# Kernel tuning notes

Measured on AMD Instinct MI355X. Metric: run time of the kernel, lower is better.

The kernel has to match this reference:

```python
import jax, jax.numpy as jnp
import numpy as np

NX = 96
N_NODES = 6 * NX * NX          # 55296 cubed-sphere grid points
N_EDGES = 4 * N_NODES          # ~4-neighbor connectivity
HID = 32
NUM_STEPS = 3


def setup_inputs() -> dict:
    key = jax.random.key(0)
    ks = jax.random.split(key, 12)
    s = 0.05
    inp = {
        "in_node_features": jax.random.normal(ks[0], (2, 6, NX, NX, 32), jnp.float32),
        "edge_relation": jax.random.normal(ks[1], (N_EDGES, 4), jnp.float32),
        "pw1": jax.random.normal(ks[2], (32, HID), jnp.float32) * s,
        "pb1": jnp.zeros((HID,), jnp.float32),
        "pw2": jax.random.normal(ks[3], (HID, HID), jnp.float32) * s,
        "pb2": jnp.zeros((HID,), jnp.float32),
        "ew1": jax.random.normal(ks[4], (4, 32), jnp.float32) * s,
        "eb1": jnp.zeros((32,), jnp.float32),
        "ew2": jax.random.normal(ks[5], (32, HID * HID), jnp.float32) * s,
        "eb2": jnp.zeros((HID * HID,), jnp.float32),
        "conv_b": jnp.zeros((HID,), jnp.float32),
        "gru_w_ih": jax.random.normal(ks[6], (3 * HID, HID), jnp.float32) * s,
        "gru_w_hh": jax.random.normal(ks[7], (3 * HID, HID), jnp.float32) * s,
        "gru_b_ih": jnp.zeros((3 * HID,), jnp.float32),
        "gru_b_hh": jnp.zeros((3 * HID,), jnp.float32),
        "edge_src": jax.random.randint(ks[8], (N_EDGES,), 0, N_NODES, jnp.int32),
        "edge_dst": jax.random.randint(ks[9], (N_EDGES,), 0, N_NODES, jnp.int32),
    }
    return inp


def reference(in_node_features, edge_relation, pw1, pb1, pw2, pb2,
              ew1, eb1, ew2, eb2, conv_b,
              gru_w_ih, gru_w_hh, gru_b_ih, gru_b_hh,
              edge_src, edge_dst):
    B, T, nx1, nx2, C = in_node_features.shape
    N = T * nx1 * nx2
    H = pw2.shape[1]

    x = in_node_features.reshape(B, N, C)
    # project_node_features: Linear -> ReLU -> Linear
    h0 = jnp.maximum(x @ pw1 + pb1, 0.0) @ pw2 + pb2          # [B, N, H]

    # edge network (same every step): Linear -> ReLU -> Linear -> [E, H, H]
    We = (jnp.maximum(edge_relation @ ew1 + eb1, 0.0) @ ew2 + eb2)
    We = We.reshape(-1, H, H)                                  # [E, H, H]

    def seg_sum(m):  # m: [E, H] -> [N, H]
        return jax.ops.segment_sum(m, edge_dst, num_segments=N)

    def step(carry, _):
        node, hidden = carry                                   # each [B, N, H]
        # NNConv: gather src feats, per-edge matmul, scatter-sum to dst
        msg = jnp.einsum('beh,eho->beo', node[:, edge_src], We)  # [B, E, H]
        agg = jax.vmap(seg_sum)(msg) + conv_b                    # [B, N, H]
        node = jnp.maximum(agg, 0.0)                             # ReLU
        # single GRU step (seq_len = 1)
        gx = node @ gru_w_ih.T + gru_b_ih                        # [B, N, 3H]
        gh = hidden @ gru_w_hh.T + gru_b_hh
        r = jax.nn.sigmoid(gx[..., :H] + gh[..., :H])
        z = jax.nn.sigmoid(gx[..., H:2 * H] + gh[..., H:2 * H])
        n = jnp.tanh(gx[..., 2 * H:] + r * gh[..., 2 * H:])
        hidden = (1.0 - z) * n + z * hidden
        return (hidden, hidden), None

    (node, _), _ = jax.lax.scan(step, (h0, h0), None, length=NUM_STEPS)
    return node.reshape(B, T, nx1, nx2, H)
```

## Files before the change

### kernel.cpp

```cpp
#include <hip/hip_runtime.h>

typedef unsigned short u16;
typedef short s16x8 __attribute__((ext_vector_type(8)));
typedef float f32x4 __attribute__((ext_vector_type(4)));
typedef float f32x2 __attribute__((ext_vector_type(2)));

#define NNODES 55296
#define NEDGES 221184
#define ROWS   110592
#define NBLK_SCAN 216

#define PK_FMA(acc, a, b) \
    asm("v_pk_fma_f32 %0, %1, %2, %0" : "+v"(acc) : "v"(a), "v"(b))

__device__ __forceinline__ u16 f2bf(float f) {
    union { float f; unsigned u; } v; v.f = f;
    unsigned r = (v.u + 0x7fffu + ((v.u >> 16) & 1u)) >> 16;
    return (u16)r;
}
__device__ __forceinline__ float bf2f(u16 u) {
    return __uint_as_float(((unsigned)u) << 16);
}

__global__ __launch_bounds__(256) void hist_kernel(
    const int* __restrict__ edst, int* __restrict__ cnt)
{
    int i = blockIdx.x * 256 + threadIdx.x;
    atomicAdd(&cnt[edst[i]], 1);
}

__global__ __launch_bounds__(256) void scan1_kernel(
    const int* __restrict__ cnt, int* __restrict__ exc, int* __restrict__ bsum)
{
    __shared__ int s[256];
    int t = threadIdx.x, g = blockIdx.x * 256 + t;
    int v = cnt[g];
    s[t] = v; __syncthreads();
#pragma unroll
    for (int d = 1; d < 256; d <<= 1) {
        int x = (t >= d) ? s[t - d] : 0;
        __syncthreads();
        s[t] += x;
        __syncthreads();
    }
    exc[g] = s[t] - v;
    if (t == 255) bsum[blockIdx.x] = s[255];
}

__global__ __launch_bounds__(256) void scan2_kernel(
    const int* __restrict__ bsum, int* __restrict__ bofs)
{
    __shared__ int s[256];
    int t = threadIdx.x;
    int v = (t < NBLK_SCAN) ? bsum[t] : 0;
    s[t] = v; __syncthreads();
#pragma unroll
    for (int d = 1; d < 256; d <<= 1) {
        int x = (t >= d) ? s[t - d] : 0;
        __syncthreads();
        s[t] += x;
        __syncthreads();
    }
    if (t < NBLK_SCAN) bofs[t] = s[t] - v;
}

__global__ __launch_bounds__(256) void scatter_kernel(
    const int* __restrict__ edst, const int* __restrict__ esrc,
    const int* __restrict__ exc, const int* __restrict__ bofs,
    int* __restrict__ cnt,
    int* __restrict__ perm, int* __restrict__ esrcp, int* __restrict__ edstp)
{
    int i = blockIdx.x * 256 + threadIdx.x;
    int d = edst[i];
    int slot = atomicSub(&cnt[d], 1) - 1;
    int pos = exc[d] + bofs[d >> 8] + slot;
    perm[pos] = i;
    esrcp[pos] = esrc[i];
    edstp[pos] = d;
}

__global__ __launch_bounds__(256) void pack_all(
    const float* __restrict__ ew2, u16* __restrict__ ew2f,
    const float* __restrict__ pw1, u16* __restrict__ pw1h, u16* __restrict__ pw1l,
    const float* __restrict__ pw2, u16* __restrict__ pw2h, u16* __restrict__ pw2l,
    const float* __restrict__ wih, u16* __restrict__ wihh, u16* __restrict__ wihl,
    const float* __restrict__ whh, u16* __restrict__ whhh, u16* __restrict__ whhl)
{
    int b = blockIdx.x;
    const float* src; u16 *hi, *lo; int ncols, trans, base;
    if (b < 128)      { src = ew2; hi = ew2f; lo = nullptr; ncols = 1024; trans = 0; base = 0;   }
    else if (b < 132) { src = pw1; hi = pw1h; lo = pw1l;    ncols = 32;   trans = 0; base = 128; }
    else if (b < 136) { src = pw2; hi = pw2h; lo = pw2l;    ncols = 32;   trans = 0; base = 132; }
    else if (b < 148) { src = wih; hi = wihh; lo = wihl;    ncols = 96;   trans = 1; base = 136; }
    else              { src = whh; hi = whhh; lo = whhl;    ncols = 96;   trans = 1; base = 148; }
    int idx = (b - base) * 256 + threadIdx.x;
    int t = idx >> 9, rr = idx & 511, lane = rr >> 3, j = rr & 7;
    int k = (lane >> 4) * 8 + j;
    int n = t * 16 + (lane & 15);
    float v = trans ? src[n * 32 + k] : src[k * ncols + n];
    u16 hb = f2bf(v);
    hi[idx] = hb;
    if (lo) lo[idx] = f2bf(v - bf2f(hb));
}

__global__ __launch_bounds__(256) void edgemlp_kernel(
    const float* __restrict__ er, const float* __restrict__ ew1,
    const float* __restrict__ eb1, const int* __restrict__ perm,
    u16* __restrict__ rbf)
{
    __shared__ float er_lds[128];
    __shared__ float w_lds[128];
    __shared__ float b_lds[32];
    int tid = threadIdx.x;
    int e32 = blockIdx.x * 32;
    if (tid < 128) {
        int e = perm[e32 + (tid >> 2)];
        er_lds[tid] = er[e * 4 + (tid & 3)];
    } else {
        w_lds[tid - 128] = ew1[tid - 128];
    }
    if (tid < 32) b_lds[tid] = eb1[tid];
    __syncthreads();
    int el0 = tid >> 5, o = tid & 31;
    float bo = b_lds[o];
    float w0 = w_lds[o], w1 = w_lds[32 + o], w2 = w_lds[64 + o], w3 = w_lds[96 + o];
#pragma unroll
    for (int i = 0; i < 4; ++i) {
        int el = el0 + i * 8;
        const float* e4 = er_lds + el * 4;
        float v = bo + e4[0] * w0 + e4[1] * w1 + e4[2] * w2 + e4[3] * w3;
        rbf[(e32 + el) * 32 + o] = f2bf(fmaxf(v, 0.f));
    }
}

__global__ __launch_bounds__(256) void nodeproj_kernel(
    const float* __restrict__ x,
    const u16* __restrict__ pw1h, const u16* __restrict__ pw1l, const float* __restrict__ pb1,
    const u16* __restrict__ pw2h, const u16* __restrict__ pw2l, const float* __restrict__ pb2,
    float* __restrict__ st_f32, float* __restrict__ agg)
{
    __shared__ alignas(16) u16 t_hi[4][512];
    __shared__ alignas(16) u16 t_lo[4][512];
    int tid = threadIdx.x, wave = tid >> 6, lane = tid & 63;
    int quad = lane >> 4, col = lane & 15;
    int row0 = (blockIdx.x * 4 + wave) * 16;

    {
        f32x4 z = {0,0,0,0};
        float* zp = agg + (size_t)(row0 + col) * 32 + quad * 8;
        *(f32x4*)(zp) = z; *(f32x4*)(zp + 4) = z;
    }

    const float* xp = x + (size_t)(row0 + col) * 32 + quad * 8;
    f32x4 xv0 = *(const f32x4*)(xp), xv1 = *(const f32x4*)(xp + 4);
    s16x8 ah, al;
#pragma unroll
    for (int i = 0; i < 4; ++i) {
        u16 h0 = f2bf(xv0[i]); ah[i] = (short)h0; al[i] = (short)f2bf(xv0[i] - bf2f(h0));
        u16 h1 = f2bf(xv1[i]); ah[4+i] = (short)h1; al[4+i] = (short)f2bf(xv1[i] - bf2f(h1));
    }
#pragma unroll
    for (int t = 0; t < 2; ++t) {
        s16x8 bh = *(const s16x8*)(pw1h + t * 512 + lane * 8);
        s16x8 bl = *(const s16x8*)(pw1l + t * 512 + lane * 8);
        f32x4 acc = {0,0,0,0};
        acc = __builtin_amdgcn_mfma_f32_16x16x32_bf16(al, bh, acc, 0,0,0);
        acc = __builtin_amdgcn_mfma_f32_16x16x32_bf16(ah, bl, acc, 0,0,0);
        acc = __builtin_amdgcn_mfma_f32_16x16x32_bf16(ah, bh, acc, 0,0,0);
        float bias = pb1[t * 16 + col];
#pragma unroll
        for (int r = 0; r < 4; ++r) {
            float v = fmaxf(acc[r] + bias, 0.f);
            u16 hb = f2bf(v);
            int idx = (quad * 4 + r) * 32 + t * 16 + col;
            t_hi[wave][idx] = hb;
            t_lo[wave][idx] = f2bf(v - bf2f(hb));
        }
    }
    __syncthreads();
    s16x8 th = *(const s16x8*)(&t_hi[wave][col * 32 + quad * 8]);
    s16x8 tl = *(const s16x8*)(&t_lo[wave][col * 32 + quad * 8]);
#pragma unroll
    for (int t = 0; t < 2; ++t) {
        s16x8 bh = *(const s16x8*)(pw2h + t * 512 + lane * 8);
        s16x8 bl = *(const s16x8*)(pw2l + t * 512 + lane * 8);
        f32x4 acc = {0,0,0,0};
        acc = __builtin_amdgcn_mfma_f32_16x16x32_bf16(tl, bh, acc, 0,0,0);
        acc = __builtin_amdgcn_mfma_f32_16x16x32_bf16(th, bl, acc, 0,0,0);
        acc = __builtin_amdgcn_mfma_f32_16x16x32_bf16(th, bh, acc, 0,0,0);
        float bias = pb2[t * 16 + col];
#pragma unroll
        for (int r = 0; r < 4; ++r) {
            float v = acc[r] + bias;
            int row = row0 + quad * 4 + r;
            int o = t * 16 + col;
            st_f32[(size_t)row * 32 + o] = v;
        }
    }
}

__global__ __launch_bounds__(256) void msg_kernel(
    const u16* __restrict__ rbf, const u16* __restrict__ ew2f,
    const float* __restrict__ eb2, const float* __restrict__ state,
    const int* __restrict__ esrcp, const int* __restrict__ edstp,
    float* __restrict__ agg)
{
    __shared__ alignas(16) float eb2_lds[1024];
    __shared__ alignas(16) float ns_lds[4][64 * 18];
    int tid = threadIdx.x;
    {
        *(f32x4*)(eb2_lds + tid * 4) = *(const f32x4*)(eb2 + tid * 4);
    }
    int wave = tid >> 6, lane = tid & 63;
    int quad = lane >> 4, col = lane & 15;
    int e0 = (blockIdx.x * 4 + wave) * 16;

    s16x8 afrag = *(const s16x8*)(rbf + (size_t)(e0 + col) * 32 + quad * 8);

    {
        int el = lane >> 2, part = lane & 3;
        int b = part >> 1, hhalf = part & 1;
        int src = esrcp[e0 + el];
        const float* sp = state + (size_t)(b * NNODES + src) * 32 + hhalf * 16;
        f32x4 a0 = *(const f32x4*)(sp + 0);
        f32x4 a1 = *(const f32x4*)(sp + 4);
        f32x4 a2 = *(const f32x4*)(sp + 8);
        f32x4 a3 = *(const f32x4*)(sp + 12);
        float* wb = &ns_lds[wave][(b * 32 + hhalf * 16) * 18 + el];
        wb[0*18] = a0.x; wb[1*18] = a0.y; wb[2*18] = a0.z; wb[3*18] = a0.w;
        wb[4*18] = a1.x; wb[5*18] = a1.y; wb[6*18] = a1.z; wb[7*18] = a1.w;
        wb[8*18] = a2.x; wb[9*18] = a2.y; wb[10*18] = a2.z; wb[11*18] = a2.w;
        wb[12*18] = a3.x; wb[13*18] = a3.y; wb[14*18] = a3.z; wb[15*18] = a3.w;
    }
    int dstid[4];
#pragma unroll
    for (int r = 0; r < 4; ++r) dstid[r] = edstp[e0 + quad * 4 + r];
    __syncthreads();

    f32x2 m[2][2][2];
#pragma unroll
    for (int b = 0; b < 2; ++b)
#pragma unroll
        for (int oh = 0; oh < 2; ++oh)
#pragma unroll
            for (int p = 0; p < 2; ++p) m[b][oh][p] = f32x2{0.f, 0.f};

    const float* nsw = &ns_lds[wave][0];
    int ep = quad * 4;
#pragma unroll 4
    for (int hh = 0; hh < 16; ++hh) {
        int h0 = hh * 2, h1 = hh * 2 + 1;
        s16x8 b0 = *(const s16x8*)(ew2f + (4 * hh + 0) * 512 + lane * 8);
        s16x8 b1 = *(const s16x8*)(ew2f + (4 * hh + 1) * 512 + lane * 8);
        s16x8 b2 = *(const s16x8*)(ew2f + (4 * hh + 2) * 512 + lane * 8);
        s16x8 b3 = *(const s16x8*)(ew2f + (4 * hh + 3) * 512 + lane * 8);
        float e00 = eb2_lds[h0 * 32 + col],  e01 = eb2_lds[h0 * 32 + 16 + col];
        float e10 = eb2_lds[h1 * 32 + col],  e11 = eb2_lds[h1 * 32 + 16 + col];
        f32x4 c0 = {e00, e00, e00, e00};
        f32x4 c1 = {e01, e01, e01, e01};
        f32x4 c2 = {e10, e10, e10, e10};
        f32x4 c3 = {e11, e11, e11, e11};
        f32x4 d0 = __builtin_amdgcn_mfma_f32_16x16x32_bf16(afrag, b0, c0, 0,0,0);
        f32x4 d1 = __builtin_amdgcn_mfma_f32_16x16x32_bf16(afrag, b1, c1, 0,0,0);
        f32x4 d2 = __builtin_amdgcn_mfma_f32_16x16x32_bf16(afrag, b2, c2, 0,0,0);
        f32x4 d3 = __builtin_amdgcn_mfma_f32_16x16x32_bf16(afrag, b3, c3, 0,0,0);
        f32x2 d0l = __builtin_shufflevector(d0, d0, 0, 1), d0h = __builtin_shufflevector(d0, d0, 2, 3);
        f32x2 d1l = __builtin_shufflevector(d1, d1, 0, 1), d1h = __builtin_shufflevector(d1, d1, 2, 3);
        f32x2 d2l = __builtin_shufflevector(d2, d2, 0, 1), d2h = __builtin_shufflevector(d2, d2, 2, 3);
        f32x2 d3l = __builtin_shufflevector(d3, d3, 0, 1), d3h = __builtin_shufflevector(d3, d3, 2, 3);
        const float* r00 = nsw + (0 * 32 + h0) * 18 + ep;
        const float* r01 = nsw + (0 * 32 + h1) * 18 + ep;
        const float* r10 = nsw + (1 * 32 + h0) * 18 + ep;
        const float* r11 = nsw + (1 * 32 + h1) * 18 + ep;
        f32x2 n00a = *(const f32x2*)(r00), n00b = *(const f32x2*)(r00 + 2);
        f32x2 n01a = *(const f32x2*)(r01), n01b = *(const f32x2*)(r01 + 2);
        f32x2 n10a = *(const f32x2*)(r10), n10b = *(const f32x2*)(r10 + 2);
        f32x2 n11a = *(const f32x2*)(r11), n11b = *(const f32x2*)(r11 + 2);
        PK_FMA(m[0][0][0], n00a, d0l); PK_FMA(m[0][0][0], n01a, d2l);
        PK_FMA(m[0][0][1], n00b, d0h); PK_FMA(m[0][0][1], n01b, d2h);
        PK_FMA(m[0][1][0], n00a, d1l); PK_FMA(m[0][1][0], n01a, d3l);
        PK_FMA(m[0][1][1], n00b, d1h); PK_FMA(m[0][1][1], n01b, d3h);
        PK_FMA(m[1][0][0], n10a, d0l); PK_FMA(m[1][0][0], n11a, d2l);
        PK_FMA(m[1][0][1], n10b, d0h); PK_FMA(m[1][0][1], n11b, d2h);
        PK_FMA(m[1][1][0], n10a, d1l); PK_FMA(m[1][1][0], n11a, d3l);
        PK_FMA(m[1][1][1], n10b, d1h); PK_FMA(m[1][1][1], n11b, d3h);
    }
    float msgs[2][2][4];
#pragma unroll
    for (int b = 0; b < 2; ++b)
#pragma unroll
        for (int oh = 0; oh < 2; ++oh) {
            msgs[b][oh][0] = m[b][oh][0].x; msgs[b][oh][1] = m[b][oh][0].y;
            msgs[b][oh][2] = m[b][oh][1].x; msgs[b][oh][3] = m[b][oh][1].y;
        }
    bool valid[4] = {true, true, true, true};
#pragma unroll
    for (int r = 3; r >= 1; --r) {
        if (dstid[r] == dstid[r - 1]) {
            valid[r] = false;
            msgs[0][0][r-1] += msgs[0][0][r];
            msgs[0][1][r-1] += msgs[0][1][r];
            msgs[1][0][r-1] += msgs[1][0][r];
            msgs[1][1][r-1] += msgs[1][1][r];
        }
    }
#pragma unroll
    for (int r = 0; r < 4; ++r) {
        if (valid[r]) {
#pragma unroll
            for (int b = 0; b < 2; ++b) {
                float* base = agg + ((size_t)b * NNODES + dstid[r]) * 32;
                unsafeAtomicAdd(base + col,      msgs[b][0][r]);
                unsafeAtomicAdd(base + 16 + col, msgs[b][1][r]);
            }
        }
    }
}

__global__ __launch_bounds__(256) void gru_kernel(
    float* __restrict__ agg, const float* __restrict__ conv_b,
    const float* __restrict__ st_f32,
    const u16* __restrict__ wihh, const u16* __restrict__ wihl,
    const u16* __restrict__ whhh, const u16* __restrict__ whhl,
    const float* __restrict__ b_ih, const float* __restrict__ b_hh,
    float* __restrict__ out_f32, int zero_agg)
{
    int tid = threadIdx.x, wave = tid >> 6, lane = tid & 63;
    int quad = lane >> 4, col = lane & 15;
    int row0 = (blockIdx.x * 4 + wave) * 16;

    float* ap = agg + (size_t)(row0 + col) * 32 + quad * 8;
    f32x4 av0 = *(const f32x4*)(ap), av1 = *(const f32x4*)(ap + 4);
    if (zero_agg) {
        f32x4 z = {0,0,0,0};
        *(f32x4*)(ap) = z; *(f32x4*)(ap + 4) = z;
    }
    const float* cb = conv_b + quad * 8;
    f32x4 cb0 = *(const f32x4*)(cb), cb1 = *(const f32x4*)(cb + 4);
    s16x8 anh, anl;
#pragma unroll
    for (int i = 0; i < 4; ++i) {
        float v0 = fmaxf(av0[i] + cb0[i], 0.f);
        float v1 = fmaxf(av1[i] + cb1[i], 0.f);
        u16 h0 = f2bf(v0); anh[i] = (short)h0;   anl[i] = (short)f2bf(v0 - bf2f(h0));
        u16 h1 = f2bf(v1); anh[4+i] = (short)h1; anl[4+i] = (short)f2bf(v1 - bf2f(h1));
    }
    const float* hp = st_f32 + (size_t)(row0 + col) * 32 + quad * 8;
    f32x4 hv0 = *(const f32x4*)(hp), hv1 = *(const f32x4*)(hp + 4);
    s16x8 ahh, ahl;
#pragma unroll
    for (int i = 0; i < 4; ++i) {
        u16 h0 = f2bf(hv0[i]); ahh[i] = (short)h0;   ahl[i] = (short)f2bf(hv0[i] - bf2f(h0));
        u16 h1 = f2bf(hv1[i]); ahh[4+i] = (short)h1; ahl[4+i] = (short)f2bf(hv1[i] - bf2f(h1));
    }

    f32x4 gx[6], gh[6];
#pragma unroll
    for (int t = 0; t < 6; ++t) {
        s16x8 bh = *(const s16x8*)(wihh + t * 512 + lane * 8);
        s16x8 bl = *(const s16x8*)(wihl + t * 512 + lane * 8);
        f32x4 acc = {0,0,0,0};
        acc = __builtin_amdgcn_mfma_f32_16x16x32_bf16(anl, bh, acc, 0,0,0);
        acc = __builtin_amdgcn_mfma_f32_16x16x32_bf16(anh, bl, acc, 0,0,0);
        acc = __builtin_amdgcn_mfma_f32_16x16x32_bf16(anh, bh, acc, 0,0,0);
        gx[t] = acc;
        s16x8 ch = *(const s16x8*)(whhh + t * 512 + lane * 8);
        s16x8 cl = *(const s16x8*)(whhl + t * 512 + lane * 8);
        f32x4 acc2 = {0,0,0,0};
        acc2 = __builtin_amdgcn_mfma_f32_16x16x32_bf16(ahl, ch, acc2, 0,0,0);
        acc2 = __builtin_amdgcn_mfma_f32_16x16x32_bf16(ahh, cl, acc2, 0,0,0);
        acc2 = __builtin_amdgcn_mfma_f32_16x16x32_bf16(ahh, ch, acc2, 0,0,0);
        gh[t] = acc2;
    }
    float bihv[6], bhhv[6];
#pragma unroll
    for (int t = 0; t < 6; ++t) { bihv[t] = b_ih[t * 16 + col]; bhhv[t] = b_hh[t * 16 + col]; }

#pragma unroll
    for (int r = 0; r < 4; ++r) {
        int row = row0 + quad * 4 + r;
#pragma unroll
        for (int oh = 0; oh < 2; ++oh) {
            int o = oh * 16 + col;
            float hid = st_f32[(size_t)row * 32 + o];
            float sr = (gx[oh][r] + bihv[oh]) + (gh[oh][r] + bhhv[oh]);
            float sz = (gx[2+oh][r] + bihv[2+oh]) + (gh[2+oh][r] + bhhv[2+oh]);
            float gxn = gx[4+oh][r] + bihv[4+oh];
            float ghn = gh[4+oh][r] + bhhv[4+oh];
            float rr = 1.f / (1.f + __expf(-sr));
            float zz = 1.f / (1.f + __expf(-sz));
            float narg = gxn + rr * ghn;
            float ex = __expf(2.f * narg);
            float nn = (ex - 1.f) / (ex + 1.f);
            float hnew = (1.f - zz) * nn + zz * hid;
            out_f32[(size_t)row * 32 + o] = hnew;
        }
    }
}

extern "C" void kernel_launch(void* const* d_in, const int* in_sizes, int n_in,
                              void* d_out, int out_size, void* d_ws, size_t ws_size,
                              hipStream_t stream)
{
    const float* x      = (const float*)d_in[0];
    const float* er     = (const float*)d_in[1];
    const float* pw1    = (const float*)d_in[2];
    const float* pb1    = (const float*)d_in[3];
    const float* pw2    = (const float*)d_in[4];
    const float* pb2    = (const float*)d_in[5];
    const float* ew1    = (const float*)d_in[6];
    const float* eb1    = (const float*)d_in[7];
    const float* ew2    = (const float*)d_in[8];
    const float* eb2    = (const float*)d_in[9];
    const float* conv_b = (const float*)d_in[10];
    const float* wih    = (const float*)d_in[11];
    const float* whh    = (const float*)d_in[12];
    const float* bih    = (const float*)d_in[13];
    const float* bhh    = (const float*)d_in[14];
    const int*   esrc   = (const int*)d_in[15];
    const int*   edst   = (const int*)d_in[16];
    float* out = (float*)d_out;

    char* ws = (char*)d_ws;
    size_t off = 0;
    auto alloc = [&](size_t bytes) -> void* {
        void* p = ws + off;
        off = (off + bytes + 255) & ~(size_t)255;
        return p;
    };
    u16*   rbf    = (u16*)  alloc((size_t)(NEDGES + 32) * 32 * 2);
    float* st_f32 = (float*)alloc((size_t)ROWS * 32 * 4);
    float* agg    = (float*)alloc((size_t)ROWS * 32 * 4);
    u16*   ew2f   = (u16*)  alloc(64 * 512 * 2);
    u16*   pw1h   = (u16*)  alloc(2 * 512 * 2);
    u16*   pw1l   = (u16*)  alloc(2 * 512 * 2);
    u16*   pw2h   = (u16*)  alloc(2 * 512 * 2);
    u16*   pw2l   = (u16*)  alloc(2 * 512 * 2);
    u16*   wihhf  = (u16*)  alloc(6 * 512 * 2);
    u16*   wihlf  = (u16*)  alloc(6 * 512 * 2);
    u16*   whhhf  = (u16*)  alloc(6 * 512 * 2);
    u16*   whhlf  = (u16*)  alloc(6 * 512 * 2);
    int*   cnt      = (int*)alloc((size_t)NNODES * 4);
    int*   exc      = (int*)alloc((size_t)NNODES * 4);
    int*   bsum     = (int*)alloc(NBLK_SCAN * 4);
    int*   bofs     = (int*)alloc(NBLK_SCAN * 4);
    int*   perm     = (int*)alloc((size_t)NEDGES * 4);
    int*   esrcp    = (int*)alloc((size_t)(NEDGES + 32) * 4);
    int*   edstp    = (int*)alloc((size_t)(NEDGES + 32) * 4);
    (void)in_sizes; (void)n_in; (void)out_size; (void)ws_size;

    hipMemsetAsync(cnt, 0, (size_t)NNODES * 4, stream);
    hist_kernel<<<NEDGES / 256, 256, 0, stream>>>(edst, cnt);
    scan1_kernel<<<NBLK_SCAN, 256, 0, stream>>>(cnt, exc, bsum);
    scan2_kernel<<<1, 256, 0, stream>>>(bsum, bofs);
    scatter_kernel<<<NEDGES / 256, 256, 0, stream>>>(edst, esrc, exc, bofs, cnt,
                                                     perm, esrcp, edstp);

    pack_all<<<160, 256, 0, stream>>>(ew2, ew2f, pw1, pw1h, pw1l, pw2, pw2h, pw2l,
                                      wih, wihhf, wihlf, whh, whhhf, whhlf);

    edgemlp_kernel<<<NEDGES / 32, 256, 0, stream>>>(er, ew1, eb1, perm, rbf);
    nodeproj_kernel<<<ROWS / 64, 256, 0, stream>>>(x, pw1h, pw1l, pb1, pw2h, pw2l, pb2,
                                                   st_f32, agg);
    for (int s = 0; s < 3; ++s) {
        msg_kernel<<<NEDGES / 64, 256, 0, stream>>>(rbf, ew2f, eb2, st_f32,
                                                    esrcp, edstp, agg);
        float* of = (s == 2) ? out : st_f32;
        gru_kernel<<<ROWS / 64, 256, 0, stream>>>(agg, conv_b, st_f32,
                                                  wihhf, wihlf, whhhf, whhlf, bih, bhh,
                                                  of, (s < 2) ? 1 : 0);
    }
}
```

Baseline: 346.2 us.

## Fuse weight packing into histogram and edge MLP into CSR scatter

Weight packing moves into the histogram kernel and the edge MLP moves into the scatter kernel, which now computes each edge's hidden row from a coalesced read and writes it straight to its sorted position. This drops two launches and the perm array with its indirect gather. It also changes the LDS layout of gathered node states in the message kernel, adding per-part offsets, which looks aimed at reducing bank conflicts. In exchange, the scatter kernel now writes 64-byte rbf rows to scattered positions.

```diff
diff --git a/kernel.cpp b/kernel.cpp
--- a/kernel.cpp
+++ b/kernel.cpp
@@ -1,9 +1,11 @@
 #include <hip/hip_runtime.h>
 
 typedef unsigned short u16;
+typedef unsigned int u32;
 typedef short s16x8 __attribute__((ext_vector_type(8)));
 typedef float f32x4 __attribute__((ext_vector_type(4)));
 typedef float f32x2 __attribute__((ext_vector_type(2)));
+typedef u32 u32x4 __attribute__((ext_vector_type(4)));
 
 #define NNODES 55296
 #define NEDGES 221184
@@ -22,11 +24,34 @@
     return __uint_as_float(((unsigned)u) << 16);
 }
 
-__global__ __launch_bounds__(256) void hist_kernel(
-    const int* __restrict__ edst, int* __restrict__ cnt)
+__global__ __launch_bounds__(256) void hist_pack_kernel(
+    const int* __restrict__ edst, int* __restrict__ cnt,
+    const float* __restrict__ ew2, u16* __restrict__ ew2f,
+    const float* __restrict__ pw1, u16* __restrict__ pw1h, u16* __restrict__ pw1l,
+    const float* __restrict__ pw2, u16* __restrict__ pw2h, u16* __restrict__ pw2l,
+    const float* __restrict__ wih, u16* __restrict__ wihh, u16* __restrict__ wihl,
+    const float* __restrict__ whh, u16* __restrict__ whhh, u16* __restrict__ whhl)
 {
     int i = blockIdx.x * 256 + threadIdx.x;
     atomicAdd(&cnt[edst[i]], 1);
+
+    int b = blockIdx.x;
+    if (b < 160) {
+        const float* src; u16 *hi, *lo; int ncols, trans, base;
+        if (b < 128)      { src = ew2; hi = ew2f; lo = nullptr; ncols = 1024; trans = 0; base = 0;   }
+        else if (b < 132) { src = pw1; hi = pw1h; lo = pw1l;    ncols = 32;   trans = 0; base = 128; }
+        else if (b < 136) { src = pw2; hi = pw2h; lo = pw2l;    ncols = 32;   trans = 0; base = 132; }
+        else if (b < 148) { src = wih; hi = wihh; lo = wihl;    ncols = 96;   trans = 1; base = 136; }
+        else              { src = whh; hi = whhh; lo = whhl;    ncols = 96;   trans = 1; base = 148; }
+        int idx = (b - base) * 256 + threadIdx.x;
+        int t = idx >> 9, rr = idx & 511, lane = rr >> 3, j = rr & 7;
+        int k = (lane >> 4) * 8 + j;
+        int n = t * 16 + (lane & 15);
+        float v = trans ? src[n * 32 + k] : src[k * ncols + n];
+        u16 hb = f2bf(v);
+        hi[idx] = hb;
+        if (lo) lo[idx] = f2bf(v - bf2f(hb));
+    }
 }
 
 __global__ __launch_bounds__(256) void scan1_kernel(
@@ -64,72 +89,46 @@
     if (t < NBLK_SCAN) bofs[t] = s[t] - v;
 }
 
-__global__ __launch_bounds__(256) void scatter_kernel(
+__global__ __launch_bounds__(256) void scatter_mlp_kernel(
     const int* __restrict__ edst, const int* __restrict__ esrc,
     const int* __restrict__ exc, const int* __restrict__ bofs,
     int* __restrict__ cnt,
-    int* __restrict__ perm, int* __restrict__ esrcp, int* __restrict__ edstp)
-{
-    int i = blockIdx.x * 256 + threadIdx.x;
+    int* __restrict__ esrcp, int* __restrict__ edstp,
+    const float* __restrict__ er, const float* __restrict__ ew1,
+    const float* __restrict__ eb1, u16* __restrict__ rbf)
+{
+    __shared__ float w_lds[128];
+    __shared__ float b_lds[32];
+    int tid = threadIdx.x;
+    if (tid < 128) w_lds[tid] = ew1[tid];
+    else if (tid < 160) b_lds[tid - 128] = eb1[tid - 128];
+    __syncthreads();
+
+    int i = blockIdx.x * 256 + tid;
     int d = edst[i];
     int slot = atomicSub(&cnt[d], 1) - 1;
     int pos = exc[d] + bofs[d >> 8] + slot;
-    perm[pos] = i;
     esrcp[pos] = esrc[i];
     edstp[pos] = d;
-}
-
-__global__ __launch_bounds__(256) void pack_all(
-    const float* __restrict__ ew2, u16* __restrict__ ew2f,
-    const float* __restrict__ pw1, u16* __restrict__ pw1h, u16* __restrict__ pw1l,
-    const float* __restrict__ pw2, u16* __restrict__ pw2h, u16* __restrict__ pw2l,
-    const float* __restrict__ wih, u16* __restrict__ wihh, u16* __restrict__ wihl,
-    const float* __restrict__ whh, u16* __restrict__ whhh, u16* __restrict__ whhl)
-{
-    int b = blockIdx.x;
-    const float* src; u16 *hi, *lo; int ncols, trans, base;
-    if (b < 128)      { src = ew2; hi = ew2f; lo = nullptr; ncols = 1024; trans = 0; base = 0;   }
-    else if (b < 132) { src = pw1; hi = pw1h; lo = pw1l;    ncols = 32;   trans = 0; base = 128; }
-    else if (b < 136) { src = pw2; hi = pw2h; lo = pw2l;    ncols = 32;   trans = 0; base = 132; }
-    else if (b < 148) { src = wih; hi = wihh; lo = wihl;    ncols = 96;   trans = 1; base = 136; }
-    else              { src = whh; hi = whhh; lo = whhl;    ncols = 96;   trans = 1; base = 148; }
-    int idx = (b - base) * 256 + threadIdx.x;
-    int t = idx >> 9, rr = idx & 511, lane = rr >> 3, j = rr & 7;
-    int k = (lane >> 4) * 8 + j;
-    int n = t * 16 + (lane & 15);
-    float v = trans ? src[n * 32 + k] : src[k * ncols + n];
-    u16 hb = f2bf(v);
-    hi[idx] = hb;
-    if (lo) lo[idx] = f2bf(v - bf2f(hb));
-}
-
-__global__ __launch_bounds__(256) void edgemlp_kernel(
-    const float* __restrict__ er, const float* __restrict__ ew1,
-    const float* __restrict__ eb1, const int* __restrict__ perm,
-    u16* __restrict__ rbf)
-{
-    __shared__ float er_lds[128];
-    __shared__ float w_lds[128];
-    __shared__ float b_lds[32];
-    int tid = threadIdx.x;
-    int e32 = blockIdx.x * 32;
-    if (tid < 128) {
-        int e = perm[e32 + (tid >> 2)];
-        er_lds[tid] = er[e * 4 + (tid & 3)];
-    } else {
-        w_lds[tid - 128] = ew1[tid - 128];
-    }
-    if (tid < 32) b_lds[tid] = eb1[tid];
-    __syncthreads();
-    int el0 = tid >> 5, o = tid & 31;
-    float bo = b_lds[o];
-    float w0 = w_lds[o], w1 = w_lds[32 + o], w2 = w_lds[64 + o], w3 = w_lds[96 + o];
-#pragma unroll
-    for (int i = 0; i < 4; ++i) {
-        int el = el0 + i * 8;
-        const float* e4 = er_lds + el * 4;
-        float v = bo + e4[0] * w0 + e4[1] * w1 + e4[2] * w2 + e4[3] * w3;
-        rbf[(e32 + el) * 32 + o] = f2bf(fmaxf(v, 0.f));
+
+    f32x4 e4 = *(const f32x4*)(er + (size_t)i * 4);
+    u32 pk[16];
+#pragma unroll
+    for (int o2 = 0; o2 < 16; ++o2) {
+        int o0 = o2 * 2, o1 = o2 * 2 + 1;
+        float v0 = b_lds[o0] + e4.x * w_lds[o0] + e4.y * w_lds[32 + o0]
+                             + e4.z * w_lds[64 + o0] + e4.w * w_lds[96 + o0];
+        float v1 = b_lds[o1] + e4.x * w_lds[o1] + e4.y * w_lds[32 + o1]
+                             + e4.z * w_lds[64 + o1] + e4.w * w_lds[96 + o1];
+        u16 h0 = f2bf(fmaxf(v0, 0.f));
+        u16 h1 = f2bf(fmaxf(v1, 0.f));
+        pk[o2] = (u32)h0 | ((u32)h1 << 16);
+    }
+    u32* dst = (u32*)(rbf + (size_t)pos * 32);
+#pragma unroll
+    for (int q = 0; q < 4; ++q) {
+        u32x4 v = {pk[q*4], pk[q*4+1], pk[q*4+2], pk[q*4+3]};
+        *(u32x4*)(dst + q * 4) = v;
     }
 }
 
@@ -206,7 +205,7 @@
     float* __restrict__ agg)
 {
     __shared__ alignas(16) float eb2_lds[1024];
-    __shared__ alignas(16) float ns_lds[4][64 * 18];
+    __shared__ alignas(16) float ns_lds[4][1200];
     int tid = threadIdx.x;
     {
         *(f32x4*)(eb2_lds + tid * 4) = *(const f32x4*)(eb2 + tid * 4);
@@ -226,7 +225,7 @@
         f32x4 a1 = *(const f32x4*)(sp + 4);
         f32x4 a2 = *(const f32x4*)(sp + 8);
         f32x4 a3 = *(const f32x4*)(sp + 12);
-        float* wb = &ns_lds[wave][(b * 32 + hhalf * 16) * 18 + el];
+        float* wb = &ns_lds[wave][(b * 32 + hhalf * 16) * 18 + part * 16 + el];
         wb[0*18] = a0.x; wb[1*18] = a0.y; wb[2*18] = a0.z; wb[3*18] = a0.w;
         wb[4*18] = a1.x; wb[5*18] = a1.y; wb[6*18] = a1.z; wb[7*18] = a1.w;
         wb[8*18] = a2.x; wb[9*18] = a2.y; wb[10*18] = a2.z; wb[11*18] = a2.w;
@@ -250,6 +249,7 @@
 #pragma unroll 4
     for (int hh = 0; hh < 16; ++hh) {
         int h0 = hh * 2, h1 = hh * 2 + 1;
+        int g = (hh >= 8) ? 1 : 0;
         s16x8 b0 = *(const s16x8*)(ew2f + (4 * hh + 0) * 512 + lane * 8);
         s16x8 b1 = *(const s16x8*)(ew2f + (4 * hh + 1) * 512 + lane * 8);
         s16x8 b2 = *(const s16x8*)(ew2f + (4 * hh + 2) * 512 + lane * 8);
@@ -268,10 +268,10 @@
         f32x2 d1l = __builtin_shufflevector(d1, d1, 0, 1), d1h = __builtin_shufflevector(d1, d1, 2, 3);
         f32x2 d2l = __builtin_shufflevector(d2, d2, 0, 1), d2h = __builtin_shufflevector(d2, d2, 2, 3);
         f32x2 d3l = __builtin_shufflevector(d3, d3, 0, 1), d3h = __builtin_shufflevector(d3, d3, 2, 3);
-        const float* r00 = nsw + (0 * 32 + h0) * 18 + ep;
-        const float* r01 = nsw + (0 * 32 + h1) * 18 + ep;
-        const float* r10 = nsw + (1 * 32 + h0) * 18 + ep;
-        const float* r11 = nsw + (1 * 32 + h1) * 18 + ep;
+        const float* r00 = nsw + h0 * 18 + g * 16 + ep;
+        const float* r01 = nsw + h1 * 18 + g * 16 + ep;
+        const float* r10 = nsw + (32 + h0) * 18 + (2 + g) * 16 + ep;
+        const float* r11 = nsw + (32 + h1) * 18 + (2 + g) * 16 + ep;
         f32x2 n00a = *(const f32x2*)(r00), n00b = *(const f32x2*)(r00 + 2);
         f32x2 n01a = *(const f32x2*)(r01), n01b = *(const f32x2*)(r01 + 2);
         f32x2 n10a = *(const f32x2*)(r10), n10b = *(const f32x2*)(r10 + 2);
@@ -444,22 +444,19 @@
     int*   exc      = (int*)alloc((size_t)NNODES * 4);
     int*   bsum     = (int*)alloc(NBLK_SCAN * 4);
     int*   bofs     = (int*)alloc(NBLK_SCAN * 4);
-    int*   perm     = (int*)alloc((size_t)NEDGES * 4);
     int*   esrcp    = (int*)alloc((size_t)(NEDGES + 32) * 4);
     int*   edstp    = (int*)alloc((size_t)(NEDGES + 32) * 4);
     (void)in_sizes; (void)n_in; (void)out_size; (void)ws_size;
 
     hipMemsetAsync(cnt, 0, (size_t)NNODES * 4, stream);
-    hist_kernel<<<NEDGES / 256, 256, 0, stream>>>(edst, cnt);
+    hist_pack_kernel<<<NEDGES / 256, 256, 0, stream>>>(
+        edst, cnt, ew2, ew2f, pw1, pw1h, pw1l, pw2, pw2h, pw2l,
+        wih, wihhf, wihlf, whh, whhhf, whhlf);
     scan1_kernel<<<NBLK_SCAN, 256, 0, stream>>>(cnt, exc, bsum);
     scan2_kernel<<<1, 256, 0, stream>>>(bsum, bofs);
-    scatter_kernel<<<NEDGES / 256, 256, 0, stream>>>(edst, esrc, exc, bofs, cnt,
-                                                     perm, esrcp, edstp);
-
-    pack_all<<<160, 256, 0, stream>>>(ew2, ew2f, pw1, pw1h, pw1l, pw2, pw2h, pw2l,
-                                      wih, wihhf, wihlf, whh, whhhf, whhlf);
-
-    edgemlp_kernel<<<NEDGES / 32, 256, 0, stream>>>(er, ew1, eb1, perm, rbf);
+    scatter_mlp_kernel<<<NEDGES / 256, 256, 0, stream>>>(
+        edst, esrc, exc, bofs, cnt, esrcp, edstp, er, ew1, eb1, rbf);
+
     nodeproj_kernel<<<ROWS / 64, 256, 0, stream>>>(x, pw1h, pw1l, pb1, pw2h, pw2l, pb2,
                                                    st_f32, agg);
     for (int s = 0; s < 3; ++s) {
```

After: 338.2 us (median of 2 runs). 2.3% less time.
